# Kernel optimization log

Hardware: AMD Instinct MI355X
Metric: run time of the kernel (lower is better)

## Reference

```python
import jax, jax.numpy as jnp
import numpy as np

D_MODEL, N_HEAD, D_FF = 768, 12, 3072
HEAD_DIM = D_MODEL // N_HEAD
EPS = 1e-5


def _layernorm(x, g, b):
    mu = jnp.mean(x, axis=-1, keepdims=True)
    var = jnp.mean((x - mu) ** 2, axis=-1, keepdims=True)
    return (x - mu) * jax.lax.rsqrt(var + EPS) * g + b


def setup_inputs() -> dict:
    key = jax.random.key(0)
    ks = jax.random.split(key, 14)
    s = 1.0 / np.sqrt(D_MODEL)
    sf = 1.0 / np.sqrt(D_FF)
    inp = {
        "x": jax.random.normal(ks[0], (2, 2048, D_MODEL), dtype=jnp.float32),
        "Wq": jax.random.normal(ks[1], (D_MODEL, D_MODEL), dtype=jnp.float32) * s,
        "bq": jnp.zeros((D_MODEL,), jnp.float32),
        "Wk": jax.random.normal(ks[2], (D_MODEL, D_MODEL), dtype=jnp.float32) * s,
        "bk": jnp.zeros((D_MODEL,), jnp.float32),
        "Wv": jax.random.normal(ks[3], (D_MODEL, D_MODEL), dtype=jnp.float32) * s,
        "bv": jnp.zeros((D_MODEL,), jnp.float32),
        "Wo": jax.random.normal(ks[4], (D_MODEL, D_MODEL), dtype=jnp.float32) * s,
        "bo": jnp.zeros((D_MODEL,), jnp.float32),
        "W1": jax.random.normal(ks[5], (D_MODEL, D_FF), dtype=jnp.float32) * s,
        "b1": jnp.zeros((D_FF,), jnp.float32),
        "W2": jax.random.normal(ks[6], (D_FF, D_MODEL), dtype=jnp.float32) * sf,
        "b2": jnp.zeros((D_MODEL,), jnp.float32),
        "ln1_g": jnp.ones((D_MODEL,), jnp.float32),
        "ln1_b": jnp.zeros((D_MODEL,), jnp.float32),
        "ln2_g": jnp.ones((D_MODEL,), jnp.float32),
        "ln2_b": jnp.zeros((D_MODEL,), jnp.float32),
    }
    return inp


def reference(x, Wq, bq, Wk, bk, Wv, bv, Wo, bo, W1, b1, W2, b2,
              ln1_g, ln1_b, ln2_g, ln2_b):
    B, S, D = x.shape
    # projections -> [B, H, S, hd]
    def proj(W, b):
        return (x @ W + b).reshape(B, S, N_HEAD, HEAD_DIM).transpose(0, 2, 1, 3)
    q, k, v = proj(Wq, bq), proj(Wk, bk), proj(Wv, bv)
    scores = jnp.einsum("bhqd,bhkd->bhqk", q, k) / jnp.sqrt(
        jnp.asarray(HEAD_DIM, jnp.float32))
    attn = jax.nn.softmax(scores, axis=-1)
    ctx = jnp.einsum("bhqk,bhkd->bhqd", attn, v)
    ctx = ctx.transpose(0, 2, 1, 3).reshape(B, S, D)
    attn_out = ctx @ Wo + bo
    h = _layernorm(x + attn_out, ln1_g, ln1_b)
    ffn = jax.nn.gelu(h @ W1 + b1, approximate=False) @ W2 + b2
    return _layernorm(h + ffn, ln2_g, ln2_b)
```

## Files before the change

### kernel.cpp

```cpp
#include <hip/hip_runtime.h>
#include <hip/hip_bf16.h>
#include <cstdint>
#include <cstddef>

typedef unsigned short u16;
typedef __bf16 bf16x8 __attribute__((ext_vector_type(8)));
typedef float f32x4 __attribute__((ext_vector_type(4)));

#define MFMA_BF16(a, b, c) __builtin_amdgcn_mfma_f32_16x16x32_bf16((a), (b), (c), 0, 0, 0)

#define GLDS16(g, l)                                                        \
  __builtin_amdgcn_global_load_lds(                                         \
      (__attribute__((address_space(1))) void*)(void*)(g),                  \
      (__attribute__((address_space(3))) void*)(void*)(l), 16, 0, 0)

#define QSCALE 0.18033688011112042f
#define PSTRIDE ((size_t)4096 * 768)

__device__ __forceinline__ u16 f2bf(float x) {
  union { float f; unsigned u; } c; c.f = x;
  unsigned u = c.u;
  unsigned r = (u + 0x7fffu + ((u >> 16) & 1u)) >> 16;
  return (u16)r;
}


__global__ __launch_bounds__(256) void transpose4_k(
    const float* __restrict__ s0, const float* __restrict__ s1,
    const float* __restrict__ s2, const float* __restrict__ s3,
    u16* __restrict__ d0, u16* __restrict__ d1,
    u16* __restrict__ d2, u16* __restrict__ d3) {
  __shared__ float tile[32][33];
  const float* in; u16* out;
  switch (blockIdx.z) {
    case 0: in = s0; out = d0; break;
    case 1: in = s1; out = d1; break;
    case 2: in = s2; out = d2; break;
    default: in = s3; out = d3; break;
  }
  const int tx = threadIdx.x & 31, ty = threadIdx.x >> 5;
  const int bx = blockIdx.x * 32, by = blockIdx.y * 32;
#pragma unroll
  for (int j = 0; j < 32; j += 8)
    tile[ty + j][tx] = in[(size_t)(by + ty + j) * 768 + bx + tx];
  __syncthreads();
#pragma unroll
  for (int j = 0; j < 32; j += 8)
    out[(size_t)(bx + ty + j) * 768 + by + tx] = f2bf(tile[tx][ty + j]);
}

__global__ __launch_bounds__(256) void transpose_bf16_k(
    const float* __restrict__ in, u16* __restrict__ out, int K, int N) {
  __shared__ float tile[32][33];
  const int tx = threadIdx.x & 31, ty = threadIdx.x >> 5;
  const int bx = blockIdx.x * 32, by = blockIdx.y * 32;
#pragma unroll
  for (int j = 0; j < 32; j += 8)
    tile[ty + j][tx] = in[(size_t)(by + ty + j) * N + bx + tx];
  __syncthreads();
#pragma unroll
  for (int j = 0; j < 32; j += 8)
    out[(size_t)(bx + ty + j) * K + by + tx] = f2bf(tile[tx][ty + j]);
}

__global__ __launch_bounds__(256) void cvt_bf16_k(
    const float* __restrict__ in, u16* __restrict__ out, int n) {
  int i = (blockIdx.x * 256 + threadIdx.x) * 4;
  if (i + 3 < n) {
    const float4 v = *(const float4*)(in + i);
    ushort4 o;
    o.x = f2bf(v.x); o.y = f2bf(v.y); o.z = f2bf(v.z); o.w = f2bf(v.w);
    *(ushort4*)(out + i) = o;
  }
}

__global__ __launch_bounds__(256) void concat3_k(
    const float* __restrict__ a, const float* __restrict__ b,
    const float* __restrict__ c, float* __restrict__ out) {
  int i = blockIdx.x * 256 + threadIdx.x;
  if (i < 768) out[i] = a[i];
  else if (i < 1536) out[i] = b[i - 768];
  else if (i < 2304) out[i] = c[i - 1536];
}

template <int EPI>
__global__ __launch_bounds__(256) void gemm_bt(
    const u16* __restrict__ A, const u16* __restrict__ BT,
    const float* __restrict__ bias, int M, int N, int K, int kchunk,
    float* __restrict__ outf, u16* __restrict__ outb,
    u16* __restrict__ qo, u16* __restrict__ ko, u16* __restrict__ vto) {
  __shared__ __align__(16) u16 lsA[128 * 64];
  __shared__ __align__(16) u16 lsB[128 * 64];
  const int tid = threadIdx.x;
  const int w = tid >> 6, lane = tid & 63;
  const int wm = w & 1, wn = w >> 1;
  const int lrow = lane & 15, quad = lane >> 4;
  const int m0 = blockIdx.y * 128, n0 = blockIdx.x * 128;
  const int kbeg = blockIdx.z * kchunk, kend = kbeg + kchunk;

  f32x4 acc[4][4];
#pragma unroll
  for (int i = 0; i < 4; ++i)
#pragma unroll
    for (int j = 0; j < 4; ++j) acc[i][j] = (f32x4){0.f, 0.f, 0.f, 0.f};

  const int off = tid * 16;
  const int srow = off >> 7;
  const int schunk = (off >> 4) & 7;
  const int sxc = schunk ^ (srow & 7);
  const int scol = sxc * 8;

  const int rsw = lrow & 7;

  for (int k0 = kbeg; k0 < kend; k0 += 64) {
    const u16* ga = A + (size_t)(m0 + srow) * K + k0 + scol;
    const u16* gb = BT + (size_t)(n0 + srow) * K + k0 + scol;
#pragma unroll
    for (int c = 0; c < 4; ++c) {
      GLDS16(ga + (size_t)(c * 32) * K, (char*)lsA + c * 4096 + off);
      GLDS16(gb + (size_t)(c * 32) * K, (char*)lsB + c * 4096 + off);
    }
    __syncthreads();
#pragma unroll
    for (int ks = 0; ks < 2; ++ks) {
      const int slot = ((ks * 4 + quad) ^ rsw) * 8;
      bf16x8 af[4], bfr[4];
#pragma unroll
      for (int ms = 0; ms < 4; ++ms)
        af[ms] = *(const bf16x8*)&lsA[(wm * 64 + ms * 16 + lrow) * 64 + slot];
#pragma unroll
      for (int ns = 0; ns < 4; ++ns)
        bfr[ns] = *(const bf16x8*)&lsB[(wn * 64 + ns * 16 + lrow) * 64 + slot];
#pragma unroll
      for (int ms = 0; ms < 4; ++ms)
#pragma unroll
        for (int ns = 0; ns < 4; ++ns)
          acc[ms][ns] = MFMA_BF16(af[ms], bfr[ns], acc[ms][ns]);
    }
    __syncthreads();
  }

  float* const pf = (EPI == 3) ? outf + (size_t)blockIdx.z * M * N : outf;
#pragma unroll
  for (int ms = 0; ms < 4; ++ms) {
    const int rbase = m0 + wm * 64 + ms * 16 + quad * 4;
#pragma unroll
    for (int ns = 0; ns < 4; ++ns) {
      const int col = n0 + wn * 64 + ns * 16 + lrow;
      if constexpr (EPI == 3) {
#pragma unroll
        for (int r = 0; r < 4; ++r)
          pf[(size_t)(rbase + r) * N + col] = acc[ms][ns][r];
      } else if constexpr (EPI == 2) {
        const float bcol = bias[col];
#pragma unroll
        for (int r = 0; r < 4; ++r) {
          float v = acc[ms][ns][r] + bcol;
          float g = 0.5f * v * (1.0f + erff(v * 0.7071067811865476f));
          outb[(size_t)(rbase + r) * N + col] = f2bf(g);
        }
      } else {
        const float bcol = bias[col];
        const int which = col / 768;
        const int rem = col - which * 768;
        const int hh = rem >> 6, dd = rem & 63;
        const int bI = rbase >> 11, sI = rbase & 2047;
        const size_t bh = (size_t)bI * 12 + hh;
        if (which == 0) {
#pragma unroll
          for (int r = 0; r < 4; ++r)
            qo[(bh * 2048 + sI + r) * 64 + dd] = f2bf((acc[ms][ns][r] + bcol) * QSCALE);
        } else if (which == 1) {
#pragma unroll
          for (int r = 0; r < 4; ++r)
            ko[(bh * 2048 + sI + r) * 64 + dd] = f2bf(acc[ms][ns][r] + bcol);
        } else {
          ushort4 pk;
          pk.x = f2bf(acc[ms][ns][0] + bcol);
          pk.y = f2bf(acc[ms][ns][1] + bcol);
          pk.z = f2bf(acc[ms][ns][2] + bcol);
          pk.w = f2bf(acc[ms][ns][3] + bcol);
          *(ushort4*)(vto + (bh * 64 + dd) * 2048 + sI) = pk;
        }
      }
    }
  }
}

__global__ __launch_bounds__(256) void attn_kernel(
    const u16* __restrict__ q, const u16* __restrict__ k,
    const u16* __restrict__ vT, u16* __restrict__ opart,
    float* __restrict__ lpart) {
  __shared__ __align__(16) u16 lsK[2 * 64 * 64];
  __shared__ __align__(16) u16 lsV[2 * 64 * 64];
  __shared__ __align__(16) u16 lsP[4][32 * 64];
  const int tid = threadIdx.x;
  const int w = tid >> 6, lane = tid & 63;
  const int lrow = lane & 15, quad = lane >> 4;
  const int bh = blockIdx.y;
  const int b = bh / 12, h = bh - b * 12;
  const int q0 = blockIdx.x * 128;
  const int z = blockIdx.z;
  const int kvbeg = z * 1024;

  const u16* qbase = q + (size_t)bh * 2048 * 64;
  const u16* kbase = k + (size_t)bh * 2048 * 64;
  const u16* vbase = vT + (size_t)bh * 64 * 2048;

  bf16x8 qf[2][2];
#pragma unroll
  for (int m = 0; m < 2; ++m) {
    const int qrow = q0 + w * 32 + m * 16 + lrow;
    qf[m][0] = *(const bf16x8*)(qbase + (size_t)qrow * 64 + quad * 8);
    qf[m][1] = *(const bf16x8*)(qbase + (size_t)qrow * 64 + 32 + quad * 8);
  }

  float lsum[2] = {0.f, 0.f};
  f32x4 oacc[2][4];
#pragma unroll
  for (int m = 0; m < 2; ++m)
#pragma unroll
    for (int d = 0; d < 4; ++d) oacc[m][d] = (f32x4){0.f, 0.f, 0.f, 0.f};

  const int off = tid * 16;
  const int srow = off >> 7;
  const int schunk = (off >> 4) & 7;
  const int sxc = schunk ^ (srow & 7);
  const int ksrc = srow * 64 + sxc * 8;
  const int vsrc0 = srow * 2048 + sxc * 8;

  const int c0 = quad ^ (lrow & 7);
  const int rd0 = c0 * 8, rd1 = (c0 ^ 4) * 8;

  u16* const lsPw = &lsP[w][0];

  auto stage = [&](int kt, int buf) {
    char* dk = (char*)(lsK + buf * 4096);
    char* dv = (char*)(lsV + buf * 4096);
    GLDS16(kbase + (size_t)kt * 64 + ksrc, dk + off);
    GLDS16(kbase + (size_t)(kt + 32) * 64 + ksrc, dk + 4096 + off);
    GLDS16(vbase + vsrc0 + kt, dv + off);
    GLDS16(vbase + vsrc0 + kt + 32 * 2048, dv + 4096 + off);
  };

  stage(kvbeg, 0);
  for (int t = 0; t < 16; ++t) {
    __syncthreads();
    if (t < 15) stage(kvbeg + (t + 1) * 64, (t + 1) & 1);
    const u16* Kb = lsK + (t & 1) * 4096;
    const u16* Vb = lsV + (t & 1) * 4096;

    f32x4 st[2][4];
#pragma unroll
    for (int js = 0; js < 4; ++js) {
      const u16* kr = Kb + (js * 16 + lrow) * 64;
      bf16x8 kf0 = *(const bf16x8*)(kr + rd0);
      bf16x8 kf1 = *(const bf16x8*)(kr + rd1);
#pragma unroll
      for (int m = 0; m < 2; ++m) {
        f32x4 s = (f32x4){0.f, 0.f, 0.f, 0.f};
        s = MFMA_BF16(kf0, qf[m][0], s);
        s = MFMA_BF16(kf1, qf[m][1], s);
        st[m][js] = s;
      }
    }

#pragma unroll
    for (int m = 0; m < 2; ++m) {
      const int mrow = m * 16 + lrow;
      u16* const prow = lsPw + mrow * 64;
      const int msw = lrow & 7;
      const int half8 = (quad & 1) * 4;
#pragma unroll
      for (int js = 0; js < 4; ++js) {
        float p0 = __builtin_amdgcn_exp2f(st[m][js][0]);
        float p1 = __builtin_amdgcn_exp2f(st[m][js][1]);
        float p2 = __builtin_amdgcn_exp2f(st[m][js][2]);
        float p3 = __builtin_amdgcn_exp2f(st[m][js][3]);
        lsum[m] += (p0 + p1) + (p2 + p3);
        union { float f; unsigned u; } u0, u1, u2, u3;
        u0.f = p0; u1.f = p1; u2.f = p2; u3.f = p3;
        ushort4 pk;
        pk.x = (u16)(u0.u >> 16); pk.y = (u16)(u1.u >> 16);
        pk.z = (u16)(u2.u >> 16); pk.w = (u16)(u3.u >> 16);
        const int cc = js * 2 + (quad >> 1);
        *(ushort4*)(prow + ((cc ^ msw) * 8) + half8) = pk;
      }
    }

#pragma unroll
    for (int d = 0; d < 4; ++d) {
      const u16* vr = Vb + (d * 16 + lrow) * 64;
      bf16x8 vf0 = *(const bf16x8*)(vr + rd0);
      bf16x8 vf1 = *(const bf16x8*)(vr + rd1);
#pragma unroll
      for (int m = 0; m < 2; ++m) {
        const u16* pr = lsPw + (m * 16 + lrow) * 64;
        bf16x8 pf0 = *(const bf16x8*)(pr + rd0);
        bf16x8 pf1 = *(const bf16x8*)(pr + rd1);
        oacc[m][d] = MFMA_BF16(pf0, vf0, oacc[m][d]);
        oacc[m][d] = MFMA_BF16(pf1, vf1, oacc[m][d]);
      }
    }
  }

#pragma unroll
  for (int m = 0; m < 2; ++m) {
    lsum[m] += __shfl_xor(lsum[m], 16);
    lsum[m] += __shfl_xor(lsum[m], 32);
  }

  u16* const op = opart + (size_t)z * PSTRIDE;
#pragma unroll
  for (int m = 0; m < 2; ++m) {
    const int srow_out = q0 + w * 32 + m * 16 + quad * 4;
#pragma unroll
    for (int d = 0; d < 4; ++d)
#pragma unroll
      for (int r = 0; r < 4; ++r)
        op[(size_t)(b * 2048 + srow_out + r) * 768 + h * 64 + d * 16 + lrow] =
            f2bf(oacc[m][d][r]);
  }
  if (quad == 0) {
#pragma unroll
    for (int m = 0; m < 2; ++m)
      lpart[(size_t)(z * 24 + bh) * 2048 + q0 + w * 32 + m * 16 + lrow] = lsum[m];
  }
}

__global__ __launch_bounds__(256) void attn_combine_k(
    const u16* __restrict__ op, const float* __restrict__ lp,
    u16* __restrict__ ctx) {
  const unsigned idx = (blockIdx.x * 256u + threadIdx.x) * 4u;
  const unsigned row = idx / 768u;
  const unsigned c = idx - row * 768u;
  const int b = row >> 11, s = row & 2047;
  const int h = c >> 6;
  const size_t li = (size_t)(b * 12 + h) * 2048 + s;
  const float rinv = 1.f / (lp[li] + lp[(size_t)24 * 2048 + li]);
  ushort4 o0 = *(const ushort4*)(op + idx);
  ushort4 o1 = *(const ushort4*)(op + PSTRIDE + idx);
  ushort4 out;
  union { unsigned u; float f; } a, bb2;
#define CMB(fld) \
  a.u = (unsigned)o0.fld << 16; bb2.u = (unsigned)o1.fld << 16; \
  out.fld = f2bf((a.f + bb2.f) * rinv);
  CMB(x) CMB(y) CMB(z) CMB(w)
#undef CMB
  *(ushort4*)(ctx + idx) = out;
}

__global__ __launch_bounds__(256) void ln_kernel(
    const float* __restrict__ parts, int nparts, const float* __restrict__ bias,
    const float* __restrict__ res, const float* __restrict__ g,
    const float* __restrict__ bb, float* __restrict__ outf, u16* __restrict__ outb) {
  const int row = blockIdx.x;
  const int tid = threadIdx.x;
  const float* pr = res + (size_t)row * 768;
  float v[3], s = 0.f, s2 = 0.f;
#pragma unroll
  for (int j = 0; j < 3; ++j) {
    const int c = tid + j * 256;
    float t = bias[c] + pr[c];
    for (int p = 0; p < nparts; ++p)
      t += parts[p * PSTRIDE + (size_t)row * 768 + c];
    v[j] = t; s += t; s2 += t * t;
  }
#pragma unroll
  for (int m = 32; m > 0; m >>= 1) {
    s += __shfl_xor(s, m);
    s2 += __shfl_xor(s2, m);
  }
  __shared__ float red[8];
  const int w = tid >> 6, lane = tid & 63;
  if (lane == 0) { red[w] = s; red[4 + w] = s2; }
  __syncthreads();
  s = red[0] + red[1] + red[2] + red[3];
  s2 = red[4] + red[5] + red[6] + red[7];
  const float mu = s * (1.f / 768.f);
  const float var = s2 * (1.f / 768.f) - mu * mu;
  const float rstd = rsqrtf(var + 1e-5f);
#pragma unroll
  for (int j = 0; j < 3; ++j) {
    const int c = tid + j * 256;
    const float y = (v[j] - mu) * rstd * g[c] + bb[c];
    if (outf) outf[(size_t)row * 768 + c] = y;
    if (outb) outb[(size_t)row * 768 + c] = f2bf(y);
  }
}

extern "C" void kernel_launch(void* const* d_in, const int* in_sizes, int n_in,
                              void* d_out, int out_size, void* d_ws, size_t ws_size,
                              hipStream_t stream) {
  const float* x    = (const float*)d_in[0];
  const float* Wq   = (const float*)d_in[1];
  const float* bq   = (const float*)d_in[2];
  const float* Wk   = (const float*)d_in[3];
  const float* bk   = (const float*)d_in[4];
  const float* Wv   = (const float*)d_in[5];
  const float* bv   = (const float*)d_in[6];
  const float* Wo   = (const float*)d_in[7];
  const float* bo   = (const float*)d_in[8];
  const float* W1   = (const float*)d_in[9];
  const float* b1   = (const float*)d_in[10];
  const float* W2   = (const float*)d_in[11];
  const float* b2   = (const float*)d_in[12];
  const float* ln1g = (const float*)d_in[13];
  const float* ln1b = (const float*)d_in[14];
  const float* ln2g = (const float*)d_in[15];
  const float* ln2b = (const float*)d_in[16];

  char* ws = (char*)d_ws;
  size_t off = 0;
  auto alloc = [&](size_t bytes) {
    void* p = ws + off;
    off += (bytes + 255) & ~(size_t)255;
    return p;
  };
  u16*  WqkvT = (u16*)alloc(2304ull * 768 * 2);
  u16*  WoT   = (u16*)alloc(768ull * 768 * 2);
  u16*  W1T   = (u16*)alloc(3072ull * 768 * 2);
  u16*  W2T   = (u16*)alloc(768ull * 3072 * 2);
  float* bqkv = (float*)alloc(2304 * 4);
  char* bigbase = (char*)alloc(0);
  u16*  xb    = (u16*)alloc(4096ull * 768 * 2);
  u16*  qb    = (u16*)alloc(24ull * 2048 * 64 * 2);
  u16*  kb    = (u16*)alloc(24ull * 2048 * 64 * 2);
  u16*  vtb   = (u16*)alloc(24ull * 64 * 2048 * 2);
  u16*  ctx   = (u16*)alloc(4096ull * 768 * 2);
  float* attno = (float*)alloc(2ull * PSTRIDE * 4);
  float* f2b   = (float*)bigbase;
  u16*   opart = (u16*)attno;
  float* lpart = (float*)((char*)attno + 2 * PSTRIDE * 2);
  float* hbuf  = (float*)alloc(4096ull * 768 * 4);
  u16*  hb    = (u16*)alloc(4096ull * 768 * 2);
  u16*  f1    = (u16*)alloc(4096ull * 3072 * 2);

  transpose4_k<<<dim3(24, 24, 4), 256, 0, stream>>>(
      Wq, Wk, Wv, Wo, WqkvT, WqkvT + 768 * 768, WqkvT + 2 * 768 * 768, WoT);
  transpose_bf16_k<<<dim3(96, 24), 256, 0, stream>>>(W1, W1T, 768, 3072);
  transpose_bf16_k<<<dim3(24, 96), 256, 0, stream>>>(W2, W2T, 3072, 768);
  concat3_k<<<9, 256, 0, stream>>>(bq, bk, bv, bqkv);
  cvt_bf16_k<<<3072, 256, 0, stream>>>(x, xb, 4096 * 768);

  gemm_bt<0><<<dim3(18, 32, 1), 256, 0, stream>>>(xb, WqkvT, bqkv, 4096, 2304, 768, 768,
                                                  nullptr, nullptr, qb, kb, vtb);
  attn_kernel<<<dim3(16, 24, 2), 256, 0, stream>>>(qb, kb, vtb, opart, lpart);
  attn_combine_k<<<3072, 256, 0, stream>>>(opart, lpart, ctx);
  gemm_bt<3><<<dim3(6, 32, 2), 256, 0, stream>>>(ctx, WoT, nullptr, 4096, 768, 768, 384,
                                                 attno, nullptr, nullptr, nullptr, nullptr);
  ln_kernel<<<4096, 256, 0, stream>>>(attno, 2, bo, x, ln1g, ln1b, hbuf, hb);
  gemm_bt<2><<<dim3(24, 32, 1), 256, 0, stream>>>(hb, W1T, b1, 4096, 3072, 768, 768,
                                                  nullptr, f1, nullptr, nullptr, nullptr);
  gemm_bt<3><<<dim3(6, 32, 4), 256, 0, stream>>>(f1, W2T, nullptr, 4096, 768, 3072, 768,
                                                 f2b, nullptr, nullptr, nullptr, nullptr);
  ln_kernel<<<4096, 256, 0, stream>>>(f2b, 4, b2, hbuf, ln2g, ln2b, (float*)d_out, nullptr);
}
```

Baseline: 323.6 us.

## Double-buffer LDS tiles in GEMM to overlap global loads with MFMA

The GEMM kernel now keeps two LDS buffers for the A and B tiles. It issues the global-to-LDS loads for the next K step before computing on the current one, and drops the second barrier per iteration. The goal is to hide global load latency behind MFMA work. In exchange LDS use doubles to 64KB per block, which may cut occupancy.

```diff
diff --git a/kernel.cpp b/kernel.cpp
--- a/kernel.cpp
+++ b/kernel.cpp
@@ -89,14 +89,14 @@
     const float* __restrict__ bias, int M, int N, int K, int kchunk,
     float* __restrict__ outf, u16* __restrict__ outb,
     u16* __restrict__ qo, u16* __restrict__ ko, u16* __restrict__ vto) {
-  __shared__ __align__(16) u16 lsA[128 * 64];
-  __shared__ __align__(16) u16 lsB[128 * 64];
+  __shared__ __align__(16) u16 lsA[2 * 128 * 64];
+  __shared__ __align__(16) u16 lsB[2 * 128 * 64];
   const int tid = threadIdx.x;
   const int w = tid >> 6, lane = tid & 63;
   const int wm = w & 1, wn = w >> 1;
   const int lrow = lane & 15, quad = lane >> 4;
   const int m0 = blockIdx.y * 128, n0 = blockIdx.x * 128;
-  const int kbeg = blockIdx.z * kchunk, kend = kbeg + kchunk;
+  const int kbeg = blockIdx.z * kchunk;
 
   f32x4 acc[4][4];
 #pragma unroll
@@ -112,32 +112,44 @@
 
   const int rsw = lrow & 7;
 
-  for (int k0 = kbeg; k0 < kend; k0 += 64) {
-    const u16* ga = A + (size_t)(m0 + srow) * K + k0 + scol;
-    const u16* gb = BT + (size_t)(n0 + srow) * K + k0 + scol;
+  const u16* ga0 = A + (size_t)(m0 + srow) * K + scol;
+  const u16* gb0 = BT + (size_t)(n0 + srow) * K + scol;
+
+  auto stage = [&](int k0, int buf) {
+    char* da = (char*)(lsA + buf * 8192);
+    char* db = (char*)(lsB + buf * 8192);
+    const u16* ga = ga0 + k0;
+    const u16* gb = gb0 + k0;
 #pragma unroll
     for (int c = 0; c < 4; ++c) {
-      GLDS16(ga + (size_t)(c * 32) * K, (char*)lsA + c * 4096 + off);
-      GLDS16(gb + (size_t)(c * 32) * K, (char*)lsB + c * 4096 + off);
-    }
+      GLDS16(ga + (size_t)(c * 32) * K, da + c * 4096 + off);
+      GLDS16(gb + (size_t)(c * 32) * K, db + c * 4096 + off);
+    }
+  };
+
+  const int niter = kchunk >> 6;
+  stage(kbeg, 0);
+  for (int t = 0; t < niter; ++t) {
     __syncthreads();
+    if (t + 1 < niter) stage(kbeg + (t + 1) * 64, (t + 1) & 1);
+    const u16* Ab = lsA + (t & 1) * 8192;
+    const u16* Bb = lsB + (t & 1) * 8192;
 #pragma unroll
     for (int ks = 0; ks < 2; ++ks) {
       const int slot = ((ks * 4 + quad) ^ rsw) * 8;
       bf16x8 af[4], bfr[4];
 #pragma unroll
       for (int ms = 0; ms < 4; ++ms)
-        af[ms] = *(const bf16x8*)&lsA[(wm * 64 + ms * 16 + lrow) * 64 + slot];
+        af[ms] = *(const bf16x8*)&Ab[(wm * 64 + ms * 16 + lrow) * 64 + slot];
 #pragma unroll
       for (int ns = 0; ns < 4; ++ns)
-        bfr[ns] = *(const bf16x8*)&lsB[(wn * 64 + ns * 16 + lrow) * 64 + slot];
+        bfr[ns] = *(const bf16x8*)&Bb[(wn * 64 + ns * 16 + lrow) * 64 + slot];
 #pragma unroll
       for (int ms = 0; ms < 4; ++ms)
 #pragma unroll
         for (int ns = 0; ns < 4; ++ns)
           acc[ms][ns] = MFMA_BF16(af[ms], bfr[ns], acc[ms][ns]);
     }
-    __syncthreads();
   }
 
   float* const pf = (EPI == 3) ? outf + (size_t)blockIdx.z * M * N : outf;
```

Result: slower. 334.7 us (+3.5%).
